# Optimization experiments

Measured on AMD Instinct MI355X. Metric: run time of the kernel, lower is better.

## Reference

```python
import jax, jax.numpy as jnp
import numpy as np

B, S, H, F, E, K = 8, 4096, 256, 512, 16, 2
EPS = 1e-5


def setup_inputs() -> dict:
    key = jax.random.key(0)
    ks = jax.random.split(key, 9)
    sc = 0.02
    return {
        "x": jax.random.normal(ks[0], (B, S, H), dtype=jnp.float32),
        "gate_w": jax.random.normal(ks[1], (H, E), dtype=jnp.float32) * sc,
        "gate_b": jnp.zeros((E,), dtype=jnp.float32),
        "w1": jax.random.normal(ks[2], (E, H, F), dtype=jnp.float32) * sc,
        "b1": jnp.zeros((E, F), dtype=jnp.float32),
        "w2": jax.random.normal(ks[3], (E, F, H), dtype=jnp.float32) * sc,
        "b2": jnp.zeros((E, H), dtype=jnp.float32),
        "gamma": jnp.ones((H,), dtype=jnp.float32),
        "beta": jnp.zeros((H,), dtype=jnp.float32),
    }


def reference(x, gate_w, gate_b, w1, b1, w2, b2, gamma, beta):
    # gating: top-k over expert logits, softmax over the k selected logits
    gate_logits = x @ gate_w + gate_b                      # [B,S,E]
    topk_vals, topk_idx = jax.lax.top_k(gate_logits, K)    # [B,S,K]
    topk_w = jax.nn.softmax(topk_vals, axis=-1)            # [B,S,K]

    # naive dense MoE: every expert runs over every token (matches source)
    h = jax.nn.relu(jnp.einsum('bsh,ehf->bsef', x, w1) + b1)   # [B,S,E,F]
    expert_out = jnp.einsum('bsef,efh->bseh', h, w2) + b2       # [B,S,E,H]

    # select top-k expert outputs and combine with gate weights
    sel = jnp.take_along_axis(expert_out, topk_idx[:, :, :, None], axis=2)  # [B,S,K,H]
    moe = jnp.sum(topk_w[..., None] * sel, axis=2)              # [B,S,H]

    # residual + LayerNorm
    y = x + moe
    mu = jnp.mean(y, axis=-1, keepdims=True)
    var = jnp.var(y, axis=-1, keepdims=True)
    return (y - mu) / jnp.sqrt(var + EPS) * gamma + beta
```

## Files before the change

### kernel.cpp

```cpp
#include <hip/hip_runtime.h>
#include <hip/hip_bf16.h>

typedef __bf16 bf16_t;
typedef __bf16 bf16x8 __attribute__((ext_vector_type(8)));
typedef __bf16 bf16x4 __attribute__((ext_vector_type(4)));
typedef float f32x4 __attribute__((ext_vector_type(4)));

#define NB 8
#define NS 4096
#define NH 256
#define NF 512
#define NE 16
#define NTOK (NB*NS)
#define TT 64
#define NCH 16
#define HS_STRIDE 40

__device__ __forceinline__ void load_lds16(const void* g, void* l) {
    __builtin_amdgcn_global_load_lds(
        (const __attribute__((address_space(1))) unsigned int*)g,
        (__attribute__((address_space(3))) unsigned int*)l, 16, 0, 0);
}

__global__ __launch_bounds__(256) void prep_kernel(
    const float* __restrict__ w1, const float* __restrict__ w2,
    bf16_t* __restrict__ w1t, bf16_t* __restrict__ w2t,
    const float* __restrict__ x, const float* __restrict__ gate_w,
    const float* __restrict__ gate_b,
    int* __restrict__ counts, int* __restrict__ bucket_enc,
    float* __restrict__ bucket_gw, bf16_t* __restrict__ xb)
{
    __shared__ float tile[32][33];
    __shared__ int lcnt[NE];
    __shared__ int gbase[NE];

    if (blockIdx.x < 128) {
        if (threadIdx.x < NE) lcnt[threadIdx.x] = 0;
        __syncthreads();

        int tok = blockIdx.x * 256 + threadIdx.x;
        const float4* xr = (const float4*)(x + (size_t)tok * NH);
        bf16x4* xbr = (bf16x4*)(xb + (size_t)tok * NH);
        float acc[NE];
        #pragma unroll
        for (int e = 0; e < NE; e++) acc[e] = gate_b[e];
        for (int h4 = 0; h4 < NH / 4; h4++) {
            float4 xv = xr[h4];
            bf16x4 xo;
            xo[0] = (bf16_t)xv.x; xo[1] = (bf16_t)xv.y;
            xo[2] = (bf16_t)xv.z; xo[3] = (bf16_t)xv.w;
            xbr[h4] = xo;
            #pragma unroll
            for (int j = 0; j < 4; j++) {
                float xs = (j == 0) ? xv.x : (j == 1) ? xv.y : (j == 2) ? xv.z : xv.w;
                const float* wr = gate_w + (h4 * 4 + j) * NE;
                #pragma unroll
                for (int e = 0; e < NE; e++) acc[e] += xs * wr[e];
            }
        }
        float v0 = -1e30f, v1 = -1e30f; int i0 = 0, i1 = 0;
        #pragma unroll
        for (int e = 0; e < NE; e++) {
            float a = acc[e];
            if (a > v0)      { v1 = v0; i1 = i0; v0 = a; i0 = e; }
            else if (a > v1) { v1 = a; i1 = e; }
        }
        float e1 = __expf(v1 - v0);
        float s  = 1.f + e1;
        int   pe[2] = { i0, i1 };
        float pg[2] = { 1.f / s, e1 / s };
        int   po[2];
        po[0] = atomicAdd(&lcnt[i0], 1);
        po[1] = atomicAdd(&lcnt[i1], 1);
        __syncthreads();
        if (threadIdx.x < NE)
            gbase[threadIdx.x] = atomicAdd(&counts[threadIdx.x], lcnt[threadIdx.x]);
        __syncthreads();
        #pragma unroll
        for (int k = 0; k < 2; k++) {
            int e = pe[k];
            int pos = gbase[e] + po[k];
            bucket_enc[e * NTOK + pos] = tok | (k << 20);
            bucket_gw [e * NTOK + pos] = pg[k];
        }
        return;
    }

    int bid = blockIdx.x - 128;
    const float* src; bf16_t* dst; int R, C; int isw1;
    if (bid < 2048) { src = w1; dst = w1t; R = NH; C = NF; isw1 = 1; }
    else            { bid -= 2048; src = w2; dst = w2t; R = NF; C = NH; isw1 = 0; }
    int e = bid >> 7;
    int t = bid & 127;
    int tcols = C / 32;
    int tr = (t / tcols) * 32, tc = (t % tcols) * 32;
    src += (size_t)e * R * C;
    dst += (size_t)e * R * C;
    int tx = threadIdx.x & 31, ty0 = threadIdx.x >> 5;
    #pragma unroll
    for (int i = 0; i < 4; i++) {
        int ty = ty0 + i * 8;
        tile[ty][tx] = src[(size_t)(tr + ty) * C + tc + tx];
    }
    __syncthreads();
    if (threadIdx.x < 128) {
        int j = threadIdx.x & 31;
        int g = threadIdx.x >> 5;
        bf16x8 v;
        #pragma unroll
        for (int jj = 0; jj < 8; jj++)
            v[jj] = (bf16_t)tile[g * 8 + jj][j];
        size_t idx;
        if (isw1) {
            int f  = tc + j;
            int kb = tr + g * 8;
            idx = (size_t)f * NH + ((((kb >> 3) ^ (f & 7))) << 3);
        } else {
            int h  = tc + j;
            int fb = tr + g * 8;
            idx = ((size_t)(fb >> 5) * NH + h) * 32 + (fb & 31);
        }
        *(bf16x8*)(dst + idx) = v;
    }
}

__global__ __launch_bounds__(256, 3) void moe_kernel(
    const bf16_t* __restrict__ xb,
    const bf16_t* __restrict__ w1t,
    const float*  __restrict__ b1,
    const bf16_t* __restrict__ w2t,
    const float*  __restrict__ b2,
    const int* __restrict__ counts,
    const int* __restrict__ bucket_enc,
    const float* __restrict__ bucket_gw,
    bf16_t* __restrict__ pairbuf,
    int* __restrict__ work_ctr)
{
    __shared__ uint4 W1s4[2][1024];
    __shared__ __align__(16) bf16_t Hs[3][TT][HS_STRIDE];
    __shared__ int   tok_s[TT];
    __shared__ float gw_s[TT];
    __shared__ float b1_s[NF];
    __shared__ float b2_s[NH];
    __shared__ int   witem_s;

    int xcd  = blockIdx.x & 7;
    int e0   = xcd * 2;
    int wave = threadIdx.x >> 6;
    int lane = threadIdx.x & 63;
    int l15 = lane & 15, q = lane >> 4;

    int n0 = counts[e0], n1 = counts[e0 + 1];
    int nt0 = (n0 + TT - 1) / TT;
    int Tpair = nt0 + (n1 + TT - 1) / TT;

    while (true) {
        if (threadIdx.x == 0) witem_s = atomicAdd(&work_ctr[xcd], 1);
        __syncthreads();
        int w = witem_s;
        if (w >= Tpair) break;
        int e, tile, n_e;
        if (w < nt0) { e = e0;     tile = w;       n_e = n0; }
        else         { e = e0 + 1; tile = w - nt0; n_e = n1; }

        const bf16_t* w1te = w1t + (size_t)e * NF * NH;
        const bf16_t* w2te = w2t + (size_t)e * NF * NH;
        int tstart = tile * TT;

        if (threadIdx.x < TT) {
            int slot = tstart + threadIdx.x;
            if (slot < n_e) {
                tok_s[threadIdx.x] = bucket_enc[e * NTOK + slot];
                gw_s [threadIdx.x] = bucket_gw [e * NTOK + slot];
            } else { tok_s[threadIdx.x] = 0; gw_s[threadIdx.x] = 0.f; }
        }
        b1_s[threadIdx.x]       = b1[e * NF + threadIdx.x];
        b1_s[threadIdx.x + 256] = b1[e * NF + threadIdx.x + 256];
        b2_s[threadIdx.x]       = b2[e * NH + threadIdx.x];
        __syncthreads();

        {
            const uint4* gw1 = (const uint4*)w1te;
            #pragma unroll
            for (int i = 0; i < 4; i++)
                load_lds16(gw1 + i * 256 + threadIdx.x, &W1s4[0][i * 256 + threadIdx.x]);
            gw1 += 1024;
            #pragma unroll
            for (int i = 0; i < 4; i++)
                load_lds16(gw1 + i * 256 + threadIdx.x, &W1s4[1][i * 256 + threadIdx.x]);
        }
        int mytok = tok_s[wave * 16 + l15] & 0xFFFFF;
        const uint4* xrow = (const uint4*)(xb + (size_t)mytok * NH);
        uint4 xf[8];
        #pragma unroll
        for (int ks = 0; ks < 8; ks++) xf[ks] = xrow[ks * 4 + q];
        bf16x8 bf2c[4], bf2n[4];
        #pragma unroll
        for (int nt = 0; nt < 4; nt++) {
            int hh = wave * 64 + nt * 16 + l15;
            bf2c[nt] = *(const bf16x8*)&w2te[((size_t)hh << 5) + q * 8];
        }
        __syncthreads();

        f32x4 oacc[4][4];
        #pragma unroll
        for (int a = 0; a < 4; a++)
            #pragma unroll
            for (int b = 0; b < 4; b++) { f32x4 z = {0.f,0.f,0.f,0.f}; oacc[a][b] = z; }

        auto gemm1 = [&](int ch, int wbuf, int hw) {
            f32x4 hacc[2]; { f32x4 z = {0.f,0.f,0.f,0.f}; hacc[0] = z; hacc[1] = z; }
            const bf16_t* w1s = (const bf16_t*)W1s4[wbuf];
            #pragma unroll
            for (int ks = 0; ks < 8; ks++) {
                bf16x8 xfrag = *(const bf16x8*)&xf[ks];
                #pragma unroll
                for (int n = 0; n < 2; n++) {
                    int fl = n * 16 + l15;
                    bf16x8 wf = *(const bf16x8*)&w1s[fl * NH + ((((ks * 4 + q) ^ (fl & 7))) << 3)];
                    hacc[n] = __builtin_amdgcn_mfma_f32_16x16x32_bf16(wf, xfrag, hacc[n], 0, 0, 0);
                }
            }
            #pragma unroll
            for (int n = 0; n < 2; n++) {
                int f0 = ch * 32 + n * 16 + q * 4;
                float4 b1v = *(const float4*)&b1_s[f0];
                bf16x4 hv;
                #pragma unroll
                for (int r = 0; r < 4; r++) {
                    float v = hacc[n][r] + ((const float*)&b1v)[r];
                    v = v > 0.f ? v : 0.f;
                    hv[r] = (bf16_t)v;
                }
                *(bf16x4*)&Hs[hw][wave * 16 + l15][n * 16 + q * 4] = hv;
            }
        };
        auto gemm2 = [&](int hr) {
            #pragma unroll
            for (int mt = 0; mt < 4; mt++) {
                bf16x8 hf = *(const bf16x8*)&Hs[hr][mt * 16 + l15][q * 8];
                #pragma unroll
                for (int nt = 0; nt < 4; nt++) {
                    oacc[mt][nt] = __builtin_amdgcn_mfma_f32_16x16x32_bf16(bf2c[nt], hf, oacc[mt][nt], 0, 0, 0);
                }
            }
        };

        gemm1(0, 0, 0);
        asm volatile("s_waitcnt lgkmcnt(0)" ::: "memory");
        __builtin_amdgcn_s_barrier();
        __builtin_amdgcn_sched_barrier(0);

        int hw = 1, hr = 0;
        for (int ch = 1; ch < NCH; ch++) {
            if (ch + 1 < NCH) {
                const uint4* gw1 = (const uint4*)w1te + (size_t)(ch + 1) * 1024;
                #pragma unroll
                for (int i = 0; i < 4; i++)
                    load_lds16(gw1 + i * 256 + threadIdx.x,
                               &W1s4[(ch + 1) & 1][i * 256 + threadIdx.x]);
            }
            #pragma unroll
            for (int nt = 0; nt < 4; nt++) {
                int hh = wave * 64 + nt * 16 + l15;
                bf2n[nt] = *(const bf16x8*)&w2te[(((size_t)ch * NH + hh) << 5) + q * 8];
            }
            gemm1(ch, ch & 1, hw);
            asm volatile("s_waitcnt vmcnt(4) lgkmcnt(0)" ::: "memory");
            __builtin_amdgcn_s_barrier();
            __builtin_amdgcn_sched_barrier(0);
            gemm2(hr);
            #pragma unroll
            for (int nt = 0; nt < 4; nt++) bf2c[nt] = bf2n[nt];
            hw = (hw == 2) ? 0 : hw + 1;
            hr = (hr == 2) ? 0 : hr + 1;
        }
        gemm2((NCH - 1) % 3);

        int nrows = n_e - tstart; if (nrows > TT) nrows = TT;
        float4 b2v[4];
        #pragma unroll
        for (int nt = 0; nt < 4; nt++)
            b2v[nt] = *(const float4*)&b2_s[wave * 64 + nt * 16 + q * 4];
        #pragma unroll
        for (int mt = 0; mt < 4; mt++) {
            int trow = mt * 16 + l15;
            int enc  = tok_s[trow];
            float gw = gw_s[trow];
            bool valid = trow < nrows;
            int tok = enc & 0xFFFFF;
            int kk  = enc >> 20;
            bf16_t* orow = pairbuf + ((size_t)(tok * 2 + kk)) * NH;
            #pragma unroll
            for (int nt = 0; nt < 4; nt++) {
                int col = wave * 64 + nt * 16 + q * 4;
                bf16x4 ov;
                #pragma unroll
                for (int r = 0; r < 4; r++)
                    ov[r] = (bf16_t)((oacc[mt][nt][r] + ((const float*)&b2v[nt])[r]) * gw);
                if (valid) *(bf16x4*)&orow[col] = ov;
            }
        }
    }
}

__global__ __launch_bounds__(256) void ln_kernel(
    const float* __restrict__ x, const bf16_t* __restrict__ pairbuf,
    const float* __restrict__ gamma, const float* __restrict__ beta,
    float* __restrict__ out)
{
    int tok  = blockIdx.x * 4 + (threadIdx.x >> 6);
    int lane = threadIdx.x & 63;
    float4 xv = *(const float4*)(x + (size_t)tok * NH + lane * 4);
    bf16x4 p0 = *(const bf16x4*)(pairbuf + (size_t)(tok * 2)     * NH + lane * 4);
    bf16x4 p1 = *(const bf16x4*)(pairbuf + (size_t)(tok * 2 + 1) * NH + lane * 4);
    float y0 = xv.x + (float)p0[0] + (float)p1[0];
    float y1 = xv.y + (float)p0[1] + (float)p1[1];
    float y2 = xv.z + (float)p0[2] + (float)p1[2];
    float y3 = xv.w + (float)p0[3] + (float)p1[3];
    float s  = y0 + y1 + y2 + y3;
    float s2 = y0 * y0 + y1 * y1 + y2 * y2 + y3 * y3;
    #pragma unroll
    for (int o = 32; o > 0; o >>= 1) {
        s  += __shfl_xor(s, o);
        s2 += __shfl_xor(s2, o);
    }
    float mu   = s * (1.f / NH);
    float var  = s2 * (1.f / NH) - mu * mu;
    float rstd = rsqrtf(var + 1e-5f);
    float4 gv = *(const float4*)(gamma + lane * 4);
    float4 bv = *(const float4*)(beta  + lane * 4);
    float4 o4;
    o4.x = (y0 - mu) * rstd * gv.x + bv.x;
    o4.y = (y1 - mu) * rstd * gv.y + bv.y;
    o4.z = (y2 - mu) * rstd * gv.z + bv.z;
    o4.w = (y3 - mu) * rstd * gv.w + bv.w;
    *(float4*)(out + (size_t)tok * NH + lane * 4) = o4;
}

extern "C" void kernel_launch(void* const* d_in, const int* in_sizes, int n_in,
                              void* d_out, int out_size, void* d_ws, size_t ws_size,
                              hipStream_t stream) {
    const float* x      = (const float*)d_in[0];
    const float* gate_w = (const float*)d_in[1];
    const float* gate_b = (const float*)d_in[2];
    const float* w1     = (const float*)d_in[3];
    const float* b1     = (const float*)d_in[4];
    const float* w2     = (const float*)d_in[5];
    const float* b2     = (const float*)d_in[6];
    const float* gamma  = (const float*)d_in[7];
    const float* beta   = (const float*)d_in[8];
    float* out = (float*)d_out;

    char* ws = (char*)d_ws;
    const size_t MB = 1024 * 1024;
    int*    counts     = (int*)ws;
    int*    work_ctr   = (int*)(ws + 128);
    int*    bucket_enc = (int*)(ws + 256);
    float*  bucket_gw  = (float*)(ws + 256 + 2 * MB);
    bf16_t* w1t        = (bf16_t*)(ws + 256 + 4 * MB);
    bf16_t* w2t        = (bf16_t*)(ws + 256 + 8 * MB);
    bf16_t* xb         = (bf16_t*)(ws + 256 + 12 * MB);
    bf16_t* pairbuf    = (bf16_t*)(ws + 256 + 28 * MB);

    hipMemsetAsync(counts, 0, 256, stream);
    prep_kernel<<<4224, 256, 0, stream>>>(w1, w2, w1t, w2t,
                                          x, gate_w, gate_b,
                                          counts, bucket_enc, bucket_gw, xb);
    moe_kernel<<<768, 256, 0, stream>>>(xb, w1t, b1, w2t, b2, counts,
                                        bucket_enc, bucket_gw, pairbuf, work_ctr);
    ln_kernel<<<NTOK / 4, 256, 0, stream>>>(x, pairbuf, gamma, beta, out);
}
```

Before: 236.0 us.

## Single-buffer W1 LDS tile to raise occupancy to four blocks per CU

The W1 staging in LDS is cut from double to single buffer and the H buffer from triple to double. This lowers LDS use so launch bounds and the grid can go to four blocks per CU (1024 blocks). The software pipeline is restructured: the next W1 chunk now loads only after gemm1 finishes, with a full vmcnt(0) wait and an extra barrier each chunk. This removes overlap between W1 loads and gemm1 inside a block, relying on more resident blocks to hide that latency.

```diff
diff --git a/kernel.cpp b/kernel.cpp
--- a/kernel.cpp
+++ b/kernel.cpp
@@ -124,7 +124,7 @@
     }
 }
 
-__global__ __launch_bounds__(256, 3) void moe_kernel(
+__global__ __launch_bounds__(256, 4) void moe_kernel(
     const bf16_t* __restrict__ xb,
     const bf16_t* __restrict__ w1t,
     const float*  __restrict__ b1,
@@ -136,8 +136,8 @@
     bf16_t* __restrict__ pairbuf,
     int* __restrict__ work_ctr)
 {
-    __shared__ uint4 W1s4[2][1024];
-    __shared__ __align__(16) bf16_t Hs[3][TT][HS_STRIDE];
+    __shared__ uint4 W1s4[1024];
+    __shared__ __align__(16) bf16_t Hs[2][TT][HS_STRIDE];
     __shared__ int   tok_s[TT];
     __shared__ float gw_s[TT];
     __shared__ float b1_s[NF];
@@ -183,11 +183,7 @@
             const uint4* gw1 = (const uint4*)w1te;
             #pragma unroll
             for (int i = 0; i < 4; i++)
-                load_lds16(gw1 + i * 256 + threadIdx.x, &W1s4[0][i * 256 + threadIdx.x]);
-            gw1 += 1024;
-            #pragma unroll
-            for (int i = 0; i < 4; i++)
-                load_lds16(gw1 + i * 256 + threadIdx.x, &W1s4[1][i * 256 + threadIdx.x]);
+                load_lds16(gw1 + i * 256 + threadIdx.x, &W1s4[i * 256 + threadIdx.x]);
         }
         int mytok = tok_s[wave * 16 + l15] & 0xFFFFF;
         const uint4* xrow = (const uint4*)(xb + (size_t)mytok * NH);
@@ -208,74 +204,66 @@
             #pragma unroll
             for (int b = 0; b < 4; b++) { f32x4 z = {0.f,0.f,0.f,0.f}; oacc[a][b] = z; }
 
-        auto gemm1 = [&](int ch, int wbuf, int hw) {
-            f32x4 hacc[2]; { f32x4 z = {0.f,0.f,0.f,0.f}; hacc[0] = z; hacc[1] = z; }
-            const bf16_t* w1s = (const bf16_t*)W1s4[wbuf];
-            #pragma unroll
-            for (int ks = 0; ks < 8; ks++) {
-                bf16x8 xfrag = *(const bf16x8*)&xf[ks];
+        for (int ch = 0; ch < NCH; ch++) {
+            int hb = ch & 1;
+            {
+                f32x4 hacc[2]; { f32x4 z = {0.f,0.f,0.f,0.f}; hacc[0] = z; hacc[1] = z; }
+                const bf16_t* w1s = (const bf16_t*)W1s4;
+                #pragma unroll
+                for (int ks = 0; ks < 8; ks++) {
+                    bf16x8 xfrag = *(const bf16x8*)&xf[ks];
+                    #pragma unroll
+                    for (int n = 0; n < 2; n++) {
+                        int fl = n * 16 + l15;
+                        bf16x8 wf = *(const bf16x8*)&w1s[fl * NH + ((((ks * 4 + q) ^ (fl & 7))) << 3)];
+                        hacc[n] = __builtin_amdgcn_mfma_f32_16x16x32_bf16(wf, xfrag, hacc[n], 0, 0, 0);
+                    }
+                }
                 #pragma unroll
                 for (int n = 0; n < 2; n++) {
-                    int fl = n * 16 + l15;
-                    bf16x8 wf = *(const bf16x8*)&w1s[fl * NH + ((((ks * 4 + q) ^ (fl & 7))) << 3)];
-                    hacc[n] = __builtin_amdgcn_mfma_f32_16x16x32_bf16(wf, xfrag, hacc[n], 0, 0, 0);
+                    int f0 = ch * 32 + n * 16 + q * 4;
+                    float4 b1v = *(const float4*)&b1_s[f0];
+                    bf16x4 hv;
+                    #pragma unroll
+                    for (int r = 0; r < 4; r++) {
+                        float v = hacc[n][r] + ((const float*)&b1v)[r];
+                        v = v > 0.f ? v : 0.f;
+                        hv[r] = (bf16_t)v;
+                    }
+                    *(bf16x4*)&Hs[hb][wave * 16 + l15][n * 16 + q * 4] = hv;
                 }
             }
-            #pragma unroll
-            for (int n = 0; n < 2; n++) {
-                int f0 = ch * 32 + n * 16 + q * 4;
-                float4 b1v = *(const float4*)&b1_s[f0];
-                bf16x4 hv;
-                #pragma unroll
-                for (int r = 0; r < 4; r++) {
-                    float v = hacc[n][r] + ((const float*)&b1v)[r];
-                    v = v > 0.f ? v : 0.f;
-                    hv[r] = (bf16_t)v;
+            asm volatile("s_waitcnt lgkmcnt(0)" ::: "memory");
+            __builtin_amdgcn_s_barrier();
+            __builtin_amdgcn_sched_barrier(0);
+            if (ch + 1 < NCH) {
+                #pragma unroll
+                for (int nt = 0; nt < 4; nt++) {
+                    int hh = wave * 64 + nt * 16 + l15;
+                    bf2n[nt] = *(const bf16x8*)&w2te[(((size_t)(ch + 1) * NH + hh) << 5) + q * 8];
                 }
-                *(bf16x4*)&Hs[hw][wave * 16 + l15][n * 16 + q * 4] = hv;
-            }
-        };
-        auto gemm2 = [&](int hr) {
+                const uint4* gw1 = (const uint4*)w1te + (size_t)(ch + 1) * 1024;
+                #pragma unroll
+                for (int i = 0; i < 4; i++)
+                    load_lds16(gw1 + i * 256 + threadIdx.x,
+                               &W1s4[i * 256 + threadIdx.x]);
+            }
             #pragma unroll
             for (int mt = 0; mt < 4; mt++) {
-                bf16x8 hf = *(const bf16x8*)&Hs[hr][mt * 16 + l15][q * 8];
+                bf16x8 hf = *(const bf16x8*)&Hs[hb][mt * 16 + l15][q * 8];
                 #pragma unroll
                 for (int nt = 0; nt < 4; nt++) {
                     oacc[mt][nt] = __builtin_amdgcn_mfma_f32_16x16x32_bf16(bf2c[nt], hf, oacc[mt][nt], 0, 0, 0);
                 }
             }
-        };
-
-        gemm1(0, 0, 0);
-        asm volatile("s_waitcnt lgkmcnt(0)" ::: "memory");
-        __builtin_amdgcn_s_barrier();
-        __builtin_amdgcn_sched_barrier(0);
-
-        int hw = 1, hr = 0;
-        for (int ch = 1; ch < NCH; ch++) {
             if (ch + 1 < NCH) {
-                const uint4* gw1 = (const uint4*)w1te + (size_t)(ch + 1) * 1024;
-                #pragma unroll
-                for (int i = 0; i < 4; i++)
-                    load_lds16(gw1 + i * 256 + threadIdx.x,
-                               &W1s4[(ch + 1) & 1][i * 256 + threadIdx.x]);
-            }
-            #pragma unroll
-            for (int nt = 0; nt < 4; nt++) {
-                int hh = wave * 64 + nt * 16 + l15;
-                bf2n[nt] = *(const bf16x8*)&w2te[(((size_t)ch * NH + hh) << 5) + q * 8];
-            }
-            gemm1(ch, ch & 1, hw);
-            asm volatile("s_waitcnt vmcnt(4) lgkmcnt(0)" ::: "memory");
-            __builtin_amdgcn_s_barrier();
-            __builtin_amdgcn_sched_barrier(0);
-            gemm2(hr);
-            #pragma unroll
-            for (int nt = 0; nt < 4; nt++) bf2c[nt] = bf2n[nt];
-            hw = (hw == 2) ? 0 : hw + 1;
-            hr = (hr == 2) ? 0 : hr + 1;
-        }
-        gemm2((NCH - 1) % 3);
+                #pragma unroll
+                for (int nt = 0; nt < 4; nt++) bf2c[nt] = bf2n[nt];
+                asm volatile("s_waitcnt vmcnt(0)" ::: "memory");
+                __builtin_amdgcn_s_barrier();
+                __builtin_amdgcn_sched_barrier(0);
+            }
+        }
 
         int nrows = n_e - tstart; if (nrows > TT) nrows = TT;
         float4 b2v[4];
@@ -367,7 +355,7 @@
     prep_kernel<<<4224, 256, 0, stream>>>(w1, w2, w1t, w2t,
                                           x, gate_w, gate_b,
                                           counts, bucket_enc, bucket_gw, xb);
-    moe_kernel<<<768, 256, 0, stream>>>(xb, w1t, b1, w2t, b2, counts,
-                                        bucket_enc, bucket_gw, pairbuf, work_ctr);
+    moe_kernel<<<1024, 256, 0, stream>>>(xb, w1t, b1, w2t, b2, counts,
+                                         bucket_enc, bucket_gw, pairbuf, work_ctr);
     ln_kernel<<<NTOK / 4, 256, 0, stream>>>(x, pairbuf, gamma, beta, out);
 }
```

Measured after the change: 323.0 us. 36.9% more time.
